# Performance work log

Measured on AMD Instinct MI355X. Metric: run time of the kernel, lower is better.

Reference implementation:

```python
import jax, jax.numpy as jnp
import numpy as np

B, S, D = 131072, 30, 4
Q = 16  # q_size for both branches
V1, V2 = 21, 11


def setup_inputs() -> dict:
    key = jax.random.key(0)
    ks = jax.random.split(key, 13)
    s = 0.5  # small init scale (~1/sqrt(in))
    inp = {
        "x": jax.random.normal(ks[0], (B, S, D), dtype=jnp.float32),
        # branch 1 (v_size=21)
        "q1_w": jax.random.normal(ks[1], (D, Q), dtype=jnp.float32) * s,
        "q1_b": jax.random.normal(ks[2], (Q,), dtype=jnp.float32) * s,
        "k1_w": jax.random.normal(ks[3], (D, Q), dtype=jnp.float32) * s,
        "k1_b": jax.random.normal(ks[4], (Q,), dtype=jnp.float32) * s,
        "v1_w": jax.random.normal(ks[5], (D, V1), dtype=jnp.float32) * s,
        "v1_b": jax.random.normal(ks[6], (V1,), dtype=jnp.float32) * s,
        # branch 2 (v_size=11)
        "q2_w": jax.random.normal(ks[7], (D, Q), dtype=jnp.float32) * s,
        "q2_b": jax.random.normal(ks[8], (Q,), dtype=jnp.float32) * s,
        "k2_w": jax.random.normal(ks[9], (D, Q), dtype=jnp.float32) * s,
        "k2_b": jax.random.normal(ks[10], (Q,), dtype=jnp.float32) * s,
        "v2_w": jax.random.normal(ks[11], (D, V2), dtype=jnp.float32) * s,
        "v2_b": jax.random.normal(ks[12], (V2,), dtype=jnp.float32) * s,
    }
    return inp


def _attn(x, qw, qb, kw, kb, vw, vb):
    # x: [B, S, D]; unscaled softmax attention + tanh (faithful to source)
    q = jnp.einsum("bsd,dq->bsq", x, qw) + qb  # [B,S,Q]
    k = jnp.einsum("bsd,dq->bsq", x, kw) + kb  # [B,S,Q]
    v = jnp.einsum("bsd,dv->bsv", x, vw) + vb  # [B,S,V]
    scores = jnp.einsum("bsq,btq->bst", q, k)  # [B,S,S], no 1/sqrt(d) scaling
    attn = jax.nn.softmax(scores, axis=-1)
    out = jnp.einsum("bst,btv->bsv", attn, v)
    return jnp.tanh(out)


def reference(x, q1_w, q1_b, k1_w, k1_b, v1_w, v1_b,
              q2_w, q2_b, k2_w, k2_b, v2_w, v2_b):
    num = _attn(x, q1_w, q1_b, k1_w, k1_b, v1_w, v1_b)  # [B,S,21]
    t = _attn(x, q2_w, q2_b, k2_w, k2_b, v2_w, v2_b)    # [B,S,11]
    return (num, t)
```

## Files before the change

### kernel.cpp

```cpp
#include <hip/hip_runtime.h>

#define SS 30
#define QQ 16
#define NV1 21
#define NV2 11
#define NVT 32
#define NBPB 2
#define ROWS (NBPB * SS)
#define THREADS 64

#define LOG2E 1.44269504088896340736f

typedef float v2f __attribute__((ext_vector_type(2)));
typedef float v4f __attribute__((ext_vector_type(4)));

__device__ __forceinline__ v2f bcast(float x) { v2f r; r.x = x; r.y = x; return r; }
__device__ __forceinline__ v2f pkfma(v2f a, v2f b, v2f c) {
    return __builtin_elementwise_fma(a, b, c);
}

__global__ __launch_bounds__(64) void precompute_consts(
    const float* __restrict__ q1w, const float* __restrict__ q1b,
    const float* __restrict__ k1w,
    const float* __restrict__ q2w, const float* __restrict__ q2b,
    const float* __restrict__ k2w,
    const float* __restrict__ v1w, const float* __restrict__ v1b,
    const float* __restrict__ v2w, const float* __restrict__ v2b,
    float* __restrict__ ws)
{
    const int tid = threadIdx.x;
    if (tid < 40) {
        const int br = tid / 20, idx = tid % 20;
        const float* qw = br ? q2w : q1w;
        const float* qb = br ? q2b : q1b;
        const float* kw = br ? k2w : k1w;
        float acc = 0.f;
        if (idx < 16) {
            const int d = idx >> 2, e = idx & 3;
            #pragma unroll
            for (int q = 0; q < QQ; ++q) acc += qw[d * QQ + q] * kw[e * QQ + q];
        } else {
            const int e = idx - 16;
            #pragma unroll
            for (int q = 0; q < QQ; ++q) acc += kw[e * QQ + q] * qb[q];
        }
        ws[tid] = acc * LOG2E;
    }
    if (tid < NVT) {
        const float s2l = 2.0f * LOG2E;
        v4f w; float b;
        if (tid < NV1) {
            w.x = v1w[tid] * s2l;          w.y = v1w[NV1 + tid] * s2l;
            w.z = v1w[2 * NV1 + tid] * s2l; w.w = v1w[3 * NV1 + tid] * s2l;
            b = v1b[tid] * s2l;
        } else {
            const int p = tid - NV1;
            w.x = v2w[p] * s2l;            w.y = v2w[NV2 + p] * s2l;
            w.z = v2w[2 * NV2 + p] * s2l;  w.w = v2w[3 * NV2 + p] * s2l;
            b = v2b[p] * s2l;
        }
        reinterpret_cast<v4f*>(ws + 40)[tid] = w;
        ws[168 + tid] = b;
    }
}

__global__ __launch_bounds__(THREADS, 8) void fused_dual_attn(
    const float* __restrict__ x, const float* __restrict__ ws,
    float* __restrict__ out1, float* __restrict__ out2)
{
    __shared__ alignas(16) float stage[ROWS * NV1];

    const int tid = threadIdx.x;
    const long long blk = blockIdx.x;
    const v4f* xgv = reinterpret_cast<const v4f*>(x) + blk * ROWS;

    v2f hp[4] = {{0.f,0.f},{0.f,0.f},{0.f,0.f},{0.f,0.f}};
    if (tid < ROWS) {
        const int batch = (tid >= SS) ? 1 : 0;
        const int boff = batch * SS;
        const v4f xr = xgv[tid];

        v2f g[4];
        #pragma unroll
        for (int e = 0; e < 4; ++e) {
            g[e].x = ws[16 + e] + xr.x * ws[e] + xr.y * ws[4 + e]
                   + xr.z * ws[8 + e] + xr.w * ws[12 + e];
            g[e].y = ws[36 + e] + xr.x * ws[20 + e] + xr.y * ws[24 + e]
                   + xr.z * ws[28 + e] + xr.w * ws[32 + e];
        }

        v2f sum = {0.f, 0.f};
        #pragma unroll
        for (int t = 0; t < SS; ++t) {
            const v4f xt = xgv[boff + t];
            const v2f bx = bcast(xt.x), by = bcast(xt.y), bz = bcast(xt.z), bw = bcast(xt.w);
            v2f s = g[3] * bw;
            s = pkfma(g[2], bz, s);
            s = pkfma(g[1], by, s);
            s = pkfma(g[0], bx, s);
            v2f p;
            p.x = __builtin_amdgcn_exp2f(s.x);
            p.y = __builtin_amdgcn_exp2f(s.y);
            sum = sum + p;
            hp[0] = pkfma(p, bx, hp[0]);
            hp[1] = pkfma(p, by, hp[1]);
            hp[2] = pkfma(p, bz, hp[2]);
            hp[3] = pkfma(p, bw, hp[3]);
        }
        v2f inv;
        inv.x = __builtin_amdgcn_rcpf(sum.x);
        inv.y = __builtin_amdgcn_rcpf(sum.y);
        #pragma unroll
        for (int e = 0; e < 4; ++e) hp[e] = hp[e] * inv;
    }

    if (tid < ROWS) {
        float* sp = stage + tid * NV1;
        #pragma unroll
        for (int o = 0; o < NV1; ++o) {
            float v = ws[168 + o];
            v = fmaf(hp[0].x, ws[40 + 4 * o + 0], v);
            v = fmaf(hp[1].x, ws[40 + 4 * o + 1], v);
            v = fmaf(hp[2].x, ws[40 + 4 * o + 2], v);
            v = fmaf(hp[3].x, ws[40 + 4 * o + 3], v);
            const float ex = __builtin_amdgcn_exp2f(v);
            sp[o] = fmaf(-2.0f, __builtin_amdgcn_rcpf(ex + 1.0f), 1.0f);
        }
    }
    __syncthreads();
    {
        const int n1 = ROWS * NV1 / 4;
        v4f* dst1 = reinterpret_cast<v4f*>(out1) + blk * n1;
        const v4f* src = reinterpret_cast<const v4f*>(stage);
        for (int i = tid; i < n1; i += THREADS)
            __builtin_nontemporal_store(src[i], dst1 + i);
    }
    __syncthreads();

    if (tid < ROWS) {
        float* sp = stage + tid * NV2;
        #pragma unroll
        for (int o = 0; o < NV2; ++o) {
            const int oo = NV1 + o;
            float v = ws[168 + oo];
            v = fmaf(hp[0].y, ws[40 + 4 * oo + 0], v);
            v = fmaf(hp[1].y, ws[40 + 4 * oo + 1], v);
            v = fmaf(hp[2].y, ws[40 + 4 * oo + 2], v);
            v = fmaf(hp[3].y, ws[40 + 4 * oo + 3], v);
            const float ex = __builtin_amdgcn_exp2f(v);
            sp[o] = fmaf(-2.0f, __builtin_amdgcn_rcpf(ex + 1.0f), 1.0f);
        }
    }
    __syncthreads();
    {
        const int n2 = ROWS * NV2 / 4;
        v4f* dst2 = reinterpret_cast<v4f*>(out2) + blk * n2;
        const v4f* src = reinterpret_cast<const v4f*>(stage);
        for (int i = tid; i < n2; i += THREADS)
            __builtin_nontemporal_store(src[i], dst2 + i);
    }
}

extern "C" void kernel_launch(void* const* d_in, const int* in_sizes, int n_in,
                              void* d_out, int out_size, void* d_ws, size_t ws_size,
                              hipStream_t stream) {
    const float* x   = (const float*)d_in[0];
    const float* q1w = (const float*)d_in[1];
    const float* q1b = (const float*)d_in[2];
    const float* k1w = (const float*)d_in[3];
    const float* v1w = (const float*)d_in[5];
    const float* v1b = (const float*)d_in[6];
    const float* q2w = (const float*)d_in[7];
    const float* q2b = (const float*)d_in[8];
    const float* k2w = (const float*)d_in[9];
    const float* v2w = (const float*)d_in[11];
    const float* v2b = (const float*)d_in[12];

    const long long B = 131072LL;
    float* out1 = (float*)d_out;
    float* out2 = out1 + B * SS * NV1;
    float* ws   = (float*)d_ws;

    precompute_consts<<<1, 64, 0, stream>>>(q1w, q1b, k1w, q2w, q2b, k2w,
                                            v1w, v1b, v2w, v2b, ws);

    const int nblocks = (int)(B / NBPB);
    fused_dual_attn<<<nblocks, THREADS, 0, stream>>>(x, ws, out1, out2);
}
```

Baseline: 135.4 us.

## Process four batches per block with two query rows per thread

Each block now handles four batch elements (120 rows) with 64 threads, and each of the 60 active threads computes two query rows (s and s+15) of the same batch. The key/value row loads from x and the broadcasts are shared between the two rows, which halves the per-row load and setup overhead and doubles the independent work in the exp2 loop. The store loops are rewritten as unrolled fixed-count loops with a tail. The cost is more registers per thread, hence the launch bound drops to 4 waves/SIMD, plus fewer blocks and a larger shared staging buffer.

```diff
diff --git a/kernel.cpp b/kernel.cpp
--- a/kernel.cpp
+++ b/kernel.cpp
@@ -5,7 +5,7 @@
 #define NV1 21
 #define NV2 11
 #define NVT 32
-#define NBPB 2
+#define NBPB 4
 #define ROWS (NBPB * SS)
 #define THREADS 64
 
@@ -64,7 +64,7 @@
     }
 }
 
-__global__ __launch_bounds__(THREADS, 8) void fused_dual_attn(
+__global__ __launch_bounds__(THREADS, 4) void fused_dual_attn(
     const float* __restrict__ x, const float* __restrict__ ws,
     float* __restrict__ out1, float* __restrict__ out2)
 {
@@ -74,57 +74,89 @@
     const long long blk = blockIdx.x;
     const v4f* xgv = reinterpret_cast<const v4f*>(x) + blk * ROWS;
 
-    v2f hp[4] = {{0.f,0.f},{0.f,0.f},{0.f,0.f},{0.f,0.f}};
-    if (tid < ROWS) {
-        const int batch = (tid >= SS) ? 1 : 0;
+    v2f hA[4] = {{0.f,0.f},{0.f,0.f},{0.f,0.f},{0.f,0.f}};
+    v2f hB[4] = {{0.f,0.f},{0.f,0.f},{0.f,0.f},{0.f,0.f}};
+    int rowA = 0, rowB = 0;
+
+    if (tid < 60) {
+        const int batch = (unsigned)tid / 15;
+        const int sA = tid - batch * 15;
+        rowA = batch * SS + sA;
+        rowB = rowA + 15;
         const int boff = batch * SS;
-        const v4f xr = xgv[tid];
-
-        v2f g[4];
+        const v4f xra = xgv[rowA];
+        const v4f xrb = xgv[rowB];
+
+        v2f gA[4], gB[4];
         #pragma unroll
         for (int e = 0; e < 4; ++e) {
-            g[e].x = ws[16 + e] + xr.x * ws[e] + xr.y * ws[4 + e]
-                   + xr.z * ws[8 + e] + xr.w * ws[12 + e];
-            g[e].y = ws[36 + e] + xr.x * ws[20 + e] + xr.y * ws[24 + e]
-                   + xr.z * ws[28 + e] + xr.w * ws[32 + e];
-        }
-
-        v2f sum = {0.f, 0.f};
+            gA[e].x = ws[16 + e] + xra.x * ws[e] + xra.y * ws[4 + e]
+                    + xra.z * ws[8 + e] + xra.w * ws[12 + e];
+            gA[e].y = ws[36 + e] + xra.x * ws[20 + e] + xra.y * ws[24 + e]
+                    + xra.z * ws[28 + e] + xra.w * ws[32 + e];
+            gB[e].x = ws[16 + e] + xrb.x * ws[e] + xrb.y * ws[4 + e]
+                    + xrb.z * ws[8 + e] + xrb.w * ws[12 + e];
+            gB[e].y = ws[36 + e] + xrb.x * ws[20 + e] + xrb.y * ws[24 + e]
+                    + xrb.z * ws[28 + e] + xrb.w * ws[32 + e];
+        }
+
+        v2f sumA = {0.f, 0.f}, sumB = {0.f, 0.f};
         #pragma unroll
         for (int t = 0; t < SS; ++t) {
             const v4f xt = xgv[boff + t];
             const v2f bx = bcast(xt.x), by = bcast(xt.y), bz = bcast(xt.z), bw = bcast(xt.w);
-            v2f s = g[3] * bw;
-            s = pkfma(g[2], bz, s);
-            s = pkfma(g[1], by, s);
-            s = pkfma(g[0], bx, s);
-            v2f p;
-            p.x = __builtin_amdgcn_exp2f(s.x);
-            p.y = __builtin_amdgcn_exp2f(s.y);
-            sum = sum + p;
-            hp[0] = pkfma(p, bx, hp[0]);
-            hp[1] = pkfma(p, by, hp[1]);
-            hp[2] = pkfma(p, bz, hp[2]);
-            hp[3] = pkfma(p, bw, hp[3]);
-        }
-        v2f inv;
-        inv.x = __builtin_amdgcn_rcpf(sum.x);
-        inv.y = __builtin_amdgcn_rcpf(sum.y);
-        #pragma unroll
-        for (int e = 0; e < 4; ++e) hp[e] = hp[e] * inv;
-    }
-
-    if (tid < ROWS) {
-        float* sp = stage + tid * NV1;
+            v2f sA2 = gA[3] * bw;
+            sA2 = pkfma(gA[2], bz, sA2);
+            sA2 = pkfma(gA[1], by, sA2);
+            sA2 = pkfma(gA[0], bx, sA2);
+            v2f sB2 = gB[3] * bw;
+            sB2 = pkfma(gB[2], bz, sB2);
+            sB2 = pkfma(gB[1], by, sB2);
+            sB2 = pkfma(gB[0], bx, sB2);
+            v2f pA, pB;
+            pA.x = __builtin_amdgcn_exp2f(sA2.x);
+            pA.y = __builtin_amdgcn_exp2f(sA2.y);
+            pB.x = __builtin_amdgcn_exp2f(sB2.x);
+            pB.y = __builtin_amdgcn_exp2f(sB2.y);
+            sumA = sumA + pA;
+            sumB = sumB + pB;
+            hA[0] = pkfma(pA, bx, hA[0]);
+            hA[1] = pkfma(pA, by, hA[1]);
+            hA[2] = pkfma(pA, bz, hA[2]);
+            hA[3] = pkfma(pA, bw, hA[3]);
+            hB[0] = pkfma(pB, bx, hB[0]);
+            hB[1] = pkfma(pB, by, hB[1]);
+            hB[2] = pkfma(pB, bz, hB[2]);
+            hB[3] = pkfma(pB, bw, hB[3]);
+        }
+        v2f invA, invB;
+        invA.x = __builtin_amdgcn_rcpf(sumA.x);
+        invA.y = __builtin_amdgcn_rcpf(sumA.y);
+        invB.x = __builtin_amdgcn_rcpf(sumB.x);
+        invB.y = __builtin_amdgcn_rcpf(sumB.y);
+        #pragma unroll
+        for (int e = 0; e < 4; ++e) { hA[e] = hA[e] * invA; hB[e] = hB[e] * invB; }
+    }
+
+    if (tid < 60) {
+        float* spA = stage + rowA * NV1;
+        float* spB = stage + rowB * NV1;
         #pragma unroll
         for (int o = 0; o < NV1; ++o) {
-            float v = ws[168 + o];
-            v = fmaf(hp[0].x, ws[40 + 4 * o + 0], v);
-            v = fmaf(hp[1].x, ws[40 + 4 * o + 1], v);
-            v = fmaf(hp[2].x, ws[40 + 4 * o + 2], v);
-            v = fmaf(hp[3].x, ws[40 + 4 * o + 3], v);
-            const float ex = __builtin_amdgcn_exp2f(v);
-            sp[o] = fmaf(-2.0f, __builtin_amdgcn_rcpf(ex + 1.0f), 1.0f);
+            float vA = ws[168 + o];
+            vA = fmaf(hA[0].x, ws[40 + 4 * o + 0], vA);
+            vA = fmaf(hA[1].x, ws[40 + 4 * o + 1], vA);
+            vA = fmaf(hA[2].x, ws[40 + 4 * o + 2], vA);
+            vA = fmaf(hA[3].x, ws[40 + 4 * o + 3], vA);
+            const float exA = __builtin_amdgcn_exp2f(vA);
+            spA[o] = fmaf(-2.0f, __builtin_amdgcn_rcpf(exA + 1.0f), 1.0f);
+            float vB = ws[168 + o];
+            vB = fmaf(hB[0].x, ws[40 + 4 * o + 0], vB);
+            vB = fmaf(hB[1].x, ws[40 + 4 * o + 1], vB);
+            vB = fmaf(hB[2].x, ws[40 + 4 * o + 2], vB);
+            vB = fmaf(hB[3].x, ws[40 + 4 * o + 3], vB);
+            const float exB = __builtin_amdgcn_exp2f(vB);
+            spB[o] = fmaf(-2.0f, __builtin_amdgcn_rcpf(exB + 1.0f), 1.0f);
         }
     }
     __syncthreads();
@@ -132,23 +164,36 @@
         const int n1 = ROWS * NV1 / 4;
         v4f* dst1 = reinterpret_cast<v4f*>(out1) + blk * n1;
         const v4f* src = reinterpret_cast<const v4f*>(stage);
-        for (int i = tid; i < n1; i += THREADS)
-            __builtin_nontemporal_store(src[i], dst1 + i);
+        #pragma unroll
+        for (int k = 0; k < n1 / THREADS; ++k)
+            __builtin_nontemporal_store(src[k * THREADS + tid], dst1 + k * THREADS + tid);
+        {
+            const int i = (n1 / THREADS) * THREADS + tid;
+            if (i < n1) __builtin_nontemporal_store(src[i], dst1 + i);
+        }
     }
     __syncthreads();
 
-    if (tid < ROWS) {
-        float* sp = stage + tid * NV2;
+    if (tid < 60) {
+        float* spA = stage + rowA * NV2;
+        float* spB = stage + rowB * NV2;
         #pragma unroll
         for (int o = 0; o < NV2; ++o) {
             const int oo = NV1 + o;
-            float v = ws[168 + oo];
-            v = fmaf(hp[0].y, ws[40 + 4 * oo + 0], v);
-            v = fmaf(hp[1].y, ws[40 + 4 * oo + 1], v);
-            v = fmaf(hp[2].y, ws[40 + 4 * oo + 2], v);
-            v = fmaf(hp[3].y, ws[40 + 4 * oo + 3], v);
-            const float ex = __builtin_amdgcn_exp2f(v);
-            sp[o] = fmaf(-2.0f, __builtin_amdgcn_rcpf(ex + 1.0f), 1.0f);
+            float vA = ws[168 + oo];
+            vA = fmaf(hA[0].y, ws[40 + 4 * oo + 0], vA);
+            vA = fmaf(hA[1].y, ws[40 + 4 * oo + 1], vA);
+            vA = fmaf(hA[2].y, ws[40 + 4 * oo + 2], vA);
+            vA = fmaf(hA[3].y, ws[40 + 4 * oo + 3], vA);
+            const float exA = __builtin_amdgcn_exp2f(vA);
+            spA[o] = fmaf(-2.0f, __builtin_amdgcn_rcpf(exA + 1.0f), 1.0f);
+            float vB = ws[168 + oo];
+            vB = fmaf(hB[0].y, ws[40 + 4 * oo + 0], vB);
+            vB = fmaf(hB[1].y, ws[40 + 4 * oo + 1], vB);
+            vB = fmaf(hB[2].y, ws[40 + 4 * oo + 2], vB);
+            vB = fmaf(hB[3].y, ws[40 + 4 * oo + 3], vB);
+            const float exB = __builtin_amdgcn_exp2f(vB);
+            spB[o] = fmaf(-2.0f, __builtin_amdgcn_rcpf(exB + 1.0f), 1.0f);
         }
     }
     __syncthreads();
@@ -156,8 +201,13 @@
         const int n2 = ROWS * NV2 / 4;
         v4f* dst2 = reinterpret_cast<v4f*>(out2) + blk * n2;
         const v4f* src = reinterpret_cast<const v4f*>(stage);
-        for (int i = tid; i < n2; i += THREADS)
-            __builtin_nontemporal_store(src[i], dst2 + i);
+        #pragma unroll
+        for (int k = 0; k < n2 / THREADS; ++k)
+            __builtin_nontemporal_store(src[k * THREADS + tid], dst2 + k * THREADS + tid);
+        {
+            const int i = (n2 / THREADS) * THREADS + tid;
+            if (i < n2) __builtin_nontemporal_store(src[i], dst2 + i);
+        }
     }
 }
 
```

After: 128.7 us (median of 2 runs). 1.05x faster.
